# Kernel optimization log

Measured on AMD Instinct MI355X. Metric: run time of the kernel, lower is better.

The kernel has to match this reference:

```python
import jax, jax.numpy as jnp
import numpy as np

UNIF_T = 2.0
EPS = 1e-12  # matches F.normalize default eps


def _l2norm(a):
    return a / jnp.maximum(jnp.linalg.norm(a, axis=-1, keepdims=True), EPS)


def setup_inputs() -> dict:
    key = jax.random.key(0)
    k1, k2, k3, k4 = jax.random.split(key, 4)
    n, d = 2048, 512
    Q, K = 3, 8192
    n_classes = 16
    x = jax.random.normal(k1, (n, d), dtype=jnp.float32)
    q_data = jax.random.normal(k2, (Q, K, d), dtype=jnp.float32)
    targets = jax.random.randint(k3, (n,), 0, n_classes, dtype=jnp.int64)
    q_targets = jax.random.randint(k4, (Q, K), 0, n_classes, dtype=jnp.int64)
    return {"x": x, "q_data": q_data, "targets": targets, "q_targets": q_targets, "order": 1}


def reference(x, q_data, targets, q_targets, order):
    # x: [n, d], q_data: [Q, K, d], targets: [n], q_targets: [Q, K]
    Q, K, _ = q_data.shape
    xn = _l2norm(x)
    qn = _l2norm(q_data)
    sim = jnp.einsum('nd,qkd->qnk', xn, qn)      # [Q, n, K]
    e = jnp.exp(-UNIF_T * (2.0 - 2.0 * sim))     # [Q, n, K]
    # mask[i, j] = targets[i] == q_targets[order, j]; masked entries of the
    # `order` queue are excluded from that row's mean.
    mask = targets[:, None] == q_targets[order][None, :]   # [n, K] bool
    total = e.sum(axis=(0, 2))                              # [n]
    masked_sum = jnp.where(mask, e[order], 0.0).sum(axis=1) # [n]
    count = (Q * K - mask.sum(axis=1)).astype(e.dtype)      # [n]
    loss = jnp.mean(jnp.log((total - masked_sum) / count))
    return loss
```

## Files before the change

kernel.cpp:

```cpp
#include <hip/hip_runtime.h>
#include <hip/hip_bf16.h>
#include <cstdint>
#include <cstddef>

#define N_ROWS 2048
#define DIM    512
#define QN     3
#define KQ     8192
#define NCOL   (QN * KQ)
#define NCLASS 16

#define BM 128
#define BN 128
#define BK 128
#define NBLK (NCOL / BN)

typedef __attribute__((ext_vector_type(4))) float f32x4;

__global__ __launch_bounds__(256) void norm_cast_kernel(
    const float* __restrict__ x, const float* __restrict__ q,
    unsigned char* __restrict__ xb, unsigned char* __restrict__ qb,
    float* __restrict__ out) {
    if (blockIdx.x == 0 && threadIdx.x == 0) out[0] = 0.f;
    int row = blockIdx.x * 4 + (threadIdx.x >> 6);
    int lane = threadIdx.x & 63;
    const float* src;
    unsigned char* dst;
    if (row < N_ROWS) {
        src = x + (size_t)row * DIM;
        dst = xb + (size_t)row * DIM;
    } else {
        src = q + (size_t)(row - N_ROWS) * DIM;
        dst = qb + (size_t)(row - N_ROWS) * DIM;
    }
    float4 v0 = ((const float4*)src)[lane * 2];
    float4 v1 = ((const float4*)src)[lane * 2 + 1];
    float ss = v0.x*v0.x + v0.y*v0.y + v0.z*v0.z + v0.w*v0.w
             + v1.x*v1.x + v1.y*v1.y + v1.z*v1.z + v1.w*v1.w;
    #pragma unroll
    for (int off = 1; off < 64; off <<= 1)
        ss += __shfl_xor(ss, off, 64);
    float inv = 16.0f / fmaxf(sqrtf(ss), 1e-12f);
    int w0 = __builtin_amdgcn_cvt_pk_fp8_f32(v0.x * inv, v0.y * inv, 0,  false);
    w0     = __builtin_amdgcn_cvt_pk_fp8_f32(v0.z * inv, v0.w * inv, w0, true);
    int w1 = __builtin_amdgcn_cvt_pk_fp8_f32(v1.x * inv, v1.y * inv, 0,  false);
    w1     = __builtin_amdgcn_cvt_pk_fp8_f32(v1.z * inv, v1.w * inv, w1, true);
    uint2 o; o.x = (unsigned)w0; o.y = (unsigned)w1;
    int r3 = (row >> 3) & 1;
    *(uint2*)(dst + ((lane * 8) ^ (r3 << 3))) = o;
}

__global__ __launch_bounds__(256) void gemm_epilogue_kernel(
    const unsigned char* __restrict__ Xb,
    const unsigned char* __restrict__ Qb,
    const int* __restrict__ targets,
    const int* __restrict__ q_targets,
    const int* __restrict__ order_p,
    float* __restrict__ P) {

    __shared__ unsigned char As[BM * BK];
    __shared__ unsigned char Bs[BN * BK];

    const int tid  = threadIdx.x;
    const int lane = tid & 63;
    const int wave = tid >> 6;
    const int wm = wave >> 1, wn = wave & 1;
    const int quad = lane >> 4;
    const int l15  = lane & 15;
    const int l7   = l15 & 7;
    const int l3   = (l15 >> 3) & 1;

    const int b    = blockIdx.x;
    const int xcd  = b & 7;
    const int g    = b >> 3;
    const int colb = (g >> 4) * 8 + xcd;
    const int rowb = g & 15;
    const int m0 = rowb * BM;
    const int n0 = colb * BN;

    f32x4 acc[4][4];
    #pragma unroll
    for (int i = 0; i < 4; i++)
        #pragma unroll
        for (int j = 0; j < 4; j++)
            acc[i][j] = (f32x4){0.f, 0.f, 0.f, 0.f};

    const int stR = (lane >> 3);
    const int stC = ((lane & 7) ^ stR) * 16;

    for (int k0 = 0; k0 < DIM; k0 += BK) {
        #pragma unroll
        for (int j = 0; j < 4; j++) {
            int chunk = wave * 4 + j;
            int R = chunk * 8 + stR;
            const unsigned char* ga = Xb + (size_t)(m0 + R) * DIM + k0 + stC;
            const unsigned char* gb = Qb + (size_t)(n0 + R) * DIM + k0 + stC;
            __builtin_amdgcn_global_load_lds(
                (const __attribute__((address_space(1))) unsigned int*)ga,
                (__attribute__((address_space(3))) unsigned int*)&As[chunk * 1024 + lane * 16],
                16, 0, 0);
            __builtin_amdgcn_global_load_lds(
                (const __attribute__((address_space(1))) unsigned int*)gb,
                (__attribute__((address_space(3))) unsigned int*)&Bs[chunk * 1024 + lane * 16],
                16, 0, 0);
        }
        __syncthreads();

        #pragma unroll
        for (int ks = 0; ks < BK; ks += 32) {
            const int sw = ((((ks >> 4) + (quad >> 1)) ^ l7) << 4)
                         + (((quad & 1) ^ l3) << 3);
            long a[4], bb[4];
            #pragma unroll
            for (int mt = 0; mt < 4; mt++)
                a[mt] = *(const long*)&As[(wm * 64 + mt * 16 + l15) * BK + sw];
            #pragma unroll
            for (int nt = 0; nt < 4; nt++)
                bb[nt] = *(const long*)&Bs[(wn * 64 + nt * 16 + l15) * BK + sw];
            #pragma unroll
            for (int mt = 0; mt < 4; mt++)
                #pragma unroll
                for (int nt = 0; nt < 4; nt++)
                    acc[mt][nt] = __builtin_amdgcn_mfma_f32_16x16x32_fp8_fp8(
                        a[mt], bb[nt], acc[mt][nt], 0, 0, 0);
        }
        __syncthreads();
    }

    const int ord  = order_p[0];
    const int qIdx = colb / (KQ / BN);
    const bool isOrd = (qIdx == ord);
    const int kbase = n0 - qIdx * KQ;

    int qtv[4] = {0, 0, 0, 0};
    if (isOrd) {
        #pragma unroll
        for (int nt = 0; nt < 4; nt++)
            qtv[nt] = q_targets[ord * KQ + kbase + wn * 64 + nt * 16 + l15];
    }

    float* red = (float*)As;

    #pragma unroll
    for (int mt = 0; mt < 4; mt++) {
        int rowl = wm * 64 + mt * 16 + quad * 4;
        int tg[4] = {0, 0, 0, 0};
        if (isOrd) {
            #pragma unroll
            for (int reg = 0; reg < 4; reg++) tg[reg] = targets[m0 + rowl + reg];
        }
        #pragma unroll
        for (int reg = 0; reg < 4; reg++) {
            float s = 0.f;
            #pragma unroll
            for (int nt = 0; nt < 4; nt++) {
                float v256 = acc[mt][nt][reg];
                float e = __expf(v256 * 0.015625f - 4.0f);
                if (isOrd && tg[reg] == qtv[nt]) e = 0.f;
                s += e;
            }
            s += __shfl_xor(s, 1, 64);
            s += __shfl_xor(s, 2, 64);
            s += __shfl_xor(s, 4, 64);
            s += __shfl_xor(s, 8, 64);
            if (l15 == 0)
                red[wn * 128 + rowl + reg] = s;
        }
    }
    __syncthreads();
    if (tid < 128)
        P[(size_t)colb * N_ROWS + m0 + tid] = red[tid] + red[128 + tid];
}

__global__ __launch_bounds__(256) void reduce_kernel(
    const float* __restrict__ P,
    const int* __restrict__ targets,
    const int* __restrict__ q_targets,
    const int* __restrict__ order_p,
    float* __restrict__ out) {
    __shared__ int hist[NCLASS];
    __shared__ float partial[4];
    int tid = threadIdx.x;
    int wave = tid >> 6, lane = tid & 63;
    if (tid < NCLASS) hist[tid] = 0;
    __syncthreads();
    int ord = order_p[0];

    int local[NCLASS];
    #pragma unroll
    for (int c = 0; c < NCLASS; c++) local[c] = 0;
    for (int i = tid; i < KQ; i += 256) {
        int v = q_targets[ord * KQ + i];
        #pragma unroll
        for (int c = 0; c < NCLASS; c++)
            local[c] += __popcll(__ballot(v == c));
    }
    if (lane == 0) {
        #pragma unroll
        for (int c = 0; c < NCLASS; c++)
            atomicAdd(&hist[c], local[c]);
    }
    __syncthreads();

    int r = blockIdx.x * 256 + tid;
    float total = 0.f;
    #pragma unroll 8
    for (int nb = 0; nb < NBLK; nb++)
        total += P[(size_t)nb * N_ROWS + r];
    float cnt = (float)(QN * KQ - hist[targets[r]]);
    float v = logf(total / cnt);

    #pragma unroll
    for (int off = 1; off < 64; off <<= 1)
        v += __shfl_xor(v, off, 64);
    if (lane == 0) partial[wave] = v;
    __syncthreads();
    if (tid == 0)
        atomicAdd(out, (partial[0] + partial[1] + partial[2] + partial[3])
                       * (1.0f / (float)N_ROWS));
}

extern "C" void kernel_launch(void* const* d_in, const int* in_sizes, int n_in,
                              void* d_out, int out_size, void* d_ws, size_t ws_size,
                              hipStream_t stream) {
    const float* x         = (const float*)d_in[0];
    const float* q         = (const float*)d_in[1];
    const int*   targets   = (const int*)d_in[2];
    const int*   q_targets = (const int*)d_in[3];
    const int*   order     = (const int*)d_in[4];
    float* out = (float*)d_out;

    char* ws = (char*)d_ws;
    float* P = (float*)ws;
    unsigned char* Xb = (unsigned char*)(ws + (size_t)NBLK * N_ROWS * 4);
    unsigned char* Qb = Xb + (size_t)N_ROWS * DIM;

    norm_cast_kernel<<<(N_ROWS + NCOL) / 4, 256, 0, stream>>>(x, q, Xb, Qb, out);

    gemm_epilogue_kernel<<<NBLK * (N_ROWS / BM), 256, 0, stream>>>(
        Xb, Qb, targets, q_targets, order, P);

    reduce_kernel<<<N_ROWS / 256, 256, 0, stream>>>(P, targets, q_targets, order, out);
}
```

Baseline: 165.2 us.

## Use 256x256 tiles with double-buffered software-pipelined fp8 GEMM over 8 waves

Enlarges the GEMM block tile to 256x256 with 512 threads and a 64-wide K step. Global-to-LDS loads go into a double buffer and are issued in quarter-tile stages interleaved with MFMA phases, using explicit vmcnt waits, barriers and setprio so loads overlap compute. The swizzle in the cast kernel and the LDS reads are changed to match the 64-byte row stride. The aim is better data reuse and hidden load latency, at the cost of more registers per thread, fewer blocks, and tricky barrier and wait ordering.

```diff
diff --git a/kernel.cpp b/kernel.cpp
--- a/kernel.cpp
+++ b/kernel.cpp
@@ -1,5 +1,4 @@
 #include <hip/hip_runtime.h>
-#include <hip/hip_bf16.h>
 #include <cstdint>
 #include <cstddef>
 
@@ -10,10 +9,11 @@
 #define NCOL   (QN * KQ)
 #define NCLASS 16
 
-#define BM 128
-#define BN 128
-#define BK 128
-#define NBLK (NCOL / BN)
+#define BM 256
+#define BN 256
+#define BKT 64
+#define NT  (DIM / BKT)
+#define NBLKP (NCOL / BN)
 
 typedef __attribute__((ext_vector_type(4))) float f32x4;
 
@@ -46,11 +46,33 @@
     int w1 = __builtin_amdgcn_cvt_pk_fp8_f32(v1.x * inv, v1.y * inv, 0,  false);
     w1     = __builtin_amdgcn_cvt_pk_fp8_f32(v1.z * inv, v1.w * inv, w1, true);
     uint2 o; o.x = (unsigned)w0; o.y = (unsigned)w1;
-    int r3 = (row >> 3) & 1;
-    *(uint2*)(dst + ((lane * 8) ^ (r3 << 3))) = o;
-}
-
-__global__ __launch_bounds__(256) void gemm_epilogue_kernel(
+    int r2 = (row >> 2) & 1;
+    *(uint2*)(dst + ((lane * 8) ^ (r2 << 3))) = o;
+}
+
+#define MF(A_, B_, C_) C_ = __builtin_amdgcn_mfma_f32_16x16x32_fp8_fp8(A_, B_, C_, 0, 0, 0)
+
+#define STAGE(h_) do {                                                          \
+    const int t_ = (h_) >> 2, bf_ = t_ & 1, ht_ = (h_) & 3;                     \
+    const int chunk_ = (ht_ & 1) * 8 + wave;           \
+    const int R_ = chunk_ * 16 + stR;                      \
+    const int k0_ = t_ * BKT;                                                   \
+    if (ht_ < 2) {                                                              \
+        __builtin_amdgcn_global_load_lds(                                       \
+            (const __attribute__((address_space(1))) unsigned int*)             \
+                (Xb + (size_t)(m0 + R_) * DIM + k0_ + stC),                     \
+            (__attribute__((address_space(3))) unsigned int*)                   \
+                &As[bf_][chunk_ * 1024 + lane * 16], 16, 0, 0);                 \
+    } else {                                                                    \
+        __builtin_amdgcn_global_load_lds(                                       \
+            (const __attribute__((address_space(1))) unsigned int*)             \
+                (Qb + (size_t)(n0 + R_) * DIM + k0_ + stC),                     \
+            (__attribute__((address_space(3))) unsigned int*)                   \
+                &Bs[bf_][chunk_ * 1024 + lane * 16], 16, 0, 0);                 \
+    }                                                                           \
+} while (0)
+
+__global__ __launch_bounds__(512) void gemm_epilogue_kernel(
     const unsigned char* __restrict__ Xb,
     const unsigned char* __restrict__ Qb,
     const int* __restrict__ targets,
@@ -58,74 +80,98 @@
     const int* __restrict__ order_p,
     float* __restrict__ P) {
 
-    __shared__ unsigned char As[BM * BK];
-    __shared__ unsigned char Bs[BN * BK];
+    __shared__ unsigned char As[2][BM * BKT];
+    __shared__ unsigned char Bs[2][BN * BKT];
 
     const int tid  = threadIdx.x;
     const int lane = tid & 63;
     const int wave = tid >> 6;
-    const int wm = wave >> 1, wn = wave & 1;
+    const int wm = wave >> 2, wn = wave & 3;
     const int quad = lane >> 4;
     const int l15  = lane & 15;
-    const int l7   = l15 & 7;
-    const int l3   = (l15 >> 3) & 1;
+    const int r3l  = l15 & 3;
+    const int r2l  = (l15 >> 2) & 1;
 
     const int b    = blockIdx.x;
     const int xcd  = b & 7;
     const int g    = b >> 3;
-    const int colb = (g >> 4) * 8 + xcd;
-    const int rowb = g & 15;
+    const int colb = (g >> 3) * 8 + xcd;
+    const int rowb = g & 7;
     const int m0 = rowb * BM;
     const int n0 = colb * BN;
 
-    f32x4 acc[4][4];
-    #pragma unroll
-    for (int i = 0; i < 4; i++)
+    f32x4 acc[8][4];
+    #pragma unroll
+    for (int i = 0; i < 8; i++)
         #pragma unroll
         for (int j = 0; j < 4; j++)
             acc[i][j] = (f32x4){0.f, 0.f, 0.f, 0.f};
 
-    const int stR = (lane >> 3);
-    const int stC = ((lane & 7) ^ stR) * 16;
-
-    for (int k0 = 0; k0 < DIM; k0 += BK) {
-        #pragma unroll
-        for (int j = 0; j < 4; j++) {
-            int chunk = wave * 4 + j;
-            int R = chunk * 8 + stR;
-            const unsigned char* ga = Xb + (size_t)(m0 + R) * DIM + k0 + stC;
-            const unsigned char* gb = Qb + (size_t)(n0 + R) * DIM + k0 + stC;
-            __builtin_amdgcn_global_load_lds(
-                (const __attribute__((address_space(1))) unsigned int*)ga,
-                (__attribute__((address_space(3))) unsigned int*)&As[chunk * 1024 + lane * 16],
-                16, 0, 0);
-            __builtin_amdgcn_global_load_lds(
-                (const __attribute__((address_space(1))) unsigned int*)gb,
-                (__attribute__((address_space(3))) unsigned int*)&Bs[chunk * 1024 + lane * 16],
-                16, 0, 0);
-        }
-        __syncthreads();
-
-        #pragma unroll
-        for (int ks = 0; ks < BK; ks += 32) {
-            const int sw = ((((ks >> 4) + (quad >> 1)) ^ l7) << 4)
-                         + (((quad & 1) ^ l3) << 3);
-            long a[4], bb[4];
-            #pragma unroll
-            for (int mt = 0; mt < 4; mt++)
-                a[mt] = *(const long*)&As[(wm * 64 + mt * 16 + l15) * BK + sw];
-            #pragma unroll
-            for (int nt = 0; nt < 4; nt++)
-                bb[nt] = *(const long*)&Bs[(wn * 64 + nt * 16 + l15) * BK + sw];
-            #pragma unroll
-            for (int mt = 0; mt < 4; mt++)
-                #pragma unroll
-                for (int nt = 0; nt < 4; nt++)
-                    acc[mt][nt] = __builtin_amdgcn_mfma_f32_16x16x32_fp8_fp8(
-                        a[mt], bb[nt], acc[mt][nt], 0, 0, 0);
-        }
-        __syncthreads();
-    }
+    const int stR = lane >> 2;
+    const int stC = ((lane & 3) ^ (stR & 3)) * 16;
+
+    const int swh = ((quad & 1) ^ r2l) << 3;
+    const int sw0 = ((((quad >> 1)    ) ^ r3l) << 4) + swh;
+    const int sw1 = ((((quad >> 1) + 2) ^ r3l) << 4) + swh;
+
+    #pragma unroll
+    for (int h = 0; h < 7; ++h) STAGE(h);
+    asm volatile("s_waitcnt vmcnt(3)" ::: "memory");
+    __builtin_amdgcn_s_barrier();
+
+    #pragma unroll
+    for (int ph = 0; ph < 32; ++ph) {
+        const int it = ph >> 3, p = ph & 7;
+        const int tt = it * 2 + (p >> 2);
+        const int q  = p & 3;
+        const int bf = tt & 1;
+        const unsigned char* Ab = &As[bf][0];
+        const unsigned char* Bb = &Bs[bf][0];
+        const int mt0 = (q >> 1) * 4, ntb = (q & 1) * 2;
+
+        long a0[2], a1[2], a2[2], a3[2], b0[2], b1[2];
+        {
+            const unsigned char* pA0 = Ab + (wm * 128 + (mt0 + 0) * 16 + l15) * BKT;
+            const unsigned char* pA1 = Ab + (wm * 128 + (mt0 + 1) * 16 + l15) * BKT;
+            const unsigned char* pA2 = Ab + (wm * 128 + (mt0 + 2) * 16 + l15) * BKT;
+            const unsigned char* pA3 = Ab + (wm * 128 + (mt0 + 3) * 16 + l15) * BKT;
+            a0[0] = *(const long*)(pA0 + sw0); a0[1] = *(const long*)(pA0 + sw1);
+            a1[0] = *(const long*)(pA1 + sw0); a1[1] = *(const long*)(pA1 + sw1);
+            a2[0] = *(const long*)(pA2 + sw0); a2[1] = *(const long*)(pA2 + sw1);
+            a3[0] = *(const long*)(pA3 + sw0); a3[1] = *(const long*)(pA3 + sw1);
+            const unsigned char* pB0 = Bb + (wn * 64 + (ntb + 0) * 16 + l15) * BKT;
+            const unsigned char* pB1 = Bb + (wn * 64 + (ntb + 1) * 16 + l15) * BKT;
+            b0[0] = *(const long*)(pB0 + sw0); b0[1] = *(const long*)(pB0 + sw1);
+            b1[0] = *(const long*)(pB1 + sw0); b1[1] = *(const long*)(pB1 + sw1);
+        }
+
+        const int hs = 7 + ph;
+        if (hs < 4 * NT) STAGE(hs);
+
+        if (q == 3) {
+            if (it == 3) asm volatile("s_waitcnt vmcnt(0)" ::: "memory");
+            else         asm volatile("s_waitcnt vmcnt(3)" ::: "memory");
+        }
+        __builtin_amdgcn_s_barrier();
+
+        __builtin_amdgcn_s_setprio(1);
+        #pragma unroll
+        for (int ks = 0; ks < 2; ++ks) {
+            MF(a0[ks], b0[ks], acc[mt0 + 0][ntb + 0]);
+            MF(a0[ks], b1[ks], acc[mt0 + 0][ntb + 1]);
+            MF(a1[ks], b0[ks], acc[mt0 + 1][ntb + 0]);
+            MF(a1[ks], b1[ks], acc[mt0 + 1][ntb + 1]);
+            MF(a2[ks], b0[ks], acc[mt0 + 2][ntb + 0]);
+            MF(a2[ks], b1[ks], acc[mt0 + 2][ntb + 1]);
+            MF(a3[ks], b0[ks], acc[mt0 + 3][ntb + 0]);
+            MF(a3[ks], b1[ks], acc[mt0 + 3][ntb + 1]);
+        }
+        __builtin_amdgcn_s_setprio(0);
+        __builtin_amdgcn_s_barrier();
+    }
+
+    __syncthreads();
+    float* red = (float*)&As[0][0];
 
     const int ord  = order_p[0];
     const int qIdx = colb / (KQ / BN);
@@ -139,11 +185,9 @@
             qtv[nt] = q_targets[ord * KQ + kbase + wn * 64 + nt * 16 + l15];
     }
 
-    float* red = (float*)As;
-
-    #pragma unroll
-    for (int mt = 0; mt < 4; mt++) {
-        int rowl = wm * 64 + mt * 16 + quad * 4;
+    #pragma unroll
+    for (int mt = 0; mt < 8; mt++) {
+        int rowl = wm * 128 + mt * 16 + quad * 4;
         int tg[4] = {0, 0, 0, 0};
         if (isOrd) {
             #pragma unroll
@@ -164,12 +208,13 @@
             s += __shfl_xor(s, 4, 64);
             s += __shfl_xor(s, 8, 64);
             if (l15 == 0)
-                red[wn * 128 + rowl + reg] = s;
-        }
-    }
-    __syncthreads();
-    if (tid < 128)
-        P[(size_t)colb * N_ROWS + m0 + tid] = red[tid] + red[128 + tid];
+                red[wn * 256 + rowl + reg] = s;
+        }
+    }
+    __syncthreads();
+    if (tid < 256)
+        P[(size_t)colb * N_ROWS + m0 + tid] =
+            red[tid] + red[256 + tid] + red[512 + tid] + red[768 + tid];
 }
 
 __global__ __launch_bounds__(256) void reduce_kernel(
@@ -205,7 +250,7 @@
     int r = blockIdx.x * 256 + tid;
     float total = 0.f;
     #pragma unroll 8
-    for (int nb = 0; nb < NBLK; nb++)
+    for (int nb = 0; nb < NBLKP; nb++)
         total += P[(size_t)nb * N_ROWS + r];
     float cnt = (float)(QN * KQ - hist[targets[r]]);
     float v = logf(total / cnt);
@@ -232,12 +277,12 @@
 
     char* ws = (char*)d_ws;
     float* P = (float*)ws;
-    unsigned char* Xb = (unsigned char*)(ws + (size_t)NBLK * N_ROWS * 4);
+    unsigned char* Xb = (unsigned char*)(ws + (size_t)NBLKP * N_ROWS * 4);
     unsigned char* Qb = Xb + (size_t)N_ROWS * DIM;
 
     norm_cast_kernel<<<(N_ROWS + NCOL) / 4, 256, 0, stream>>>(x, q, Xb, Qb, out);
 
-    gemm_epilogue_kernel<<<NBLK * (N_ROWS / BM), 256, 0, stream>>>(
+    gemm_epilogue_kernel<<<NBLKP * (N_ROWS / BM), 512, 0, stream>>>(
         Xb, Qb, targets, q_targets, order, P);
 
     reduce_kernel<<<N_ROWS / 256, 256, 0, stream>>>(P, targets, q_targets, order, out);
```

Measured after the change: 191.5 us. 1.16x slower.
